# Kernel tuning notes

Measured on AMD Instinct MI355X. Metric: run time of the kernel, lower is better.

## Reference

```python
import jax, jax.numpy as jnp
import numpy as np

B, L_IN, C_IN, C_SKIP, C_OUT, DEPTH = 8, 512, 512, 512, 512, 4
D_INNER, D_STATE, D_CONV, DT_RANK = 1024, 16, 4, 32
EPS = 1e-5


def rmsnorm(x, w):
    return x * jax.lax.rsqrt(jnp.mean(x * x, axis=-1, keepdims=True) + EPS) * w


def layernorm(x, w, b):
    m = jnp.mean(x, axis=-1, keepdims=True)
    v = jnp.mean((x - m) ** 2, axis=-1, keepdims=True)
    return (x - m) * jax.lax.rsqrt(v + EPS) * w + b


def selective_scan(u, dt, A, Bm, Cm, Dp):
    # u, dt: (B, L, Di); A: (Di, N); Bm, Cm: (B, L, N); Dp: (Di,)
    def step(h, inp):
        dt_t, B_t, C_t, u_t = inp  # (B,Di),(B,N),(B,N),(B,Di)
        dA = jnp.exp(dt_t[..., None] * A)            # (B,Di,N)
        h = dA * h + (dt_t * u_t)[..., None] * B_t[:, None, :]
        y = jnp.einsum('bdn,bn->bd', h, C_t)
        return h, y

    Bb, L, Di = u.shape
    h0 = jnp.zeros((Bb, Di, A.shape[1]), u.dtype)
    xs = (dt.transpose(1, 0, 2), Bm.transpose(1, 0, 2),
          Cm.transpose(1, 0, 2), u.transpose(1, 0, 2))
    _, ys = jax.lax.scan(step, h0, xs)               # ys: (L,B,Di)
    return ys.transpose(1, 0, 2) + u * Dp


def mamba_block(x, in_w, cw, cb, xp_w, dtw, dtb, A_log, Dp, ow, ob):
    xz = x @ in_w.T                                   # (B,L,2*Di)
    xc, z = jnp.split(xz, 2, axis=-1)
    # causal depthwise conv, kernel D_CONV
    xc_t = jax.lax.conv_general_dilated(
        xc.transpose(0, 2, 1), cw[:, None, :], (1,), [(D_CONV - 1, 0)],
        feature_group_count=D_INNER,
        dimension_numbers=('NCH', 'OIH', 'NCH'))
    xc = jax.nn.silu((xc_t + cb[None, :, None]).transpose(0, 2, 1))
    xdbc = xc @ xp_w.T                                # (B,L,DT_RANK+2N)
    dtp = xdbc[..., :DT_RANK]
    Bm = xdbc[..., DT_RANK:DT_RANK + D_STATE]
    Cm = xdbc[..., DT_RANK + D_STATE:]
    dt = jax.nn.softplus(dtp @ dtw.T + dtb)
    A = -jnp.exp(A_log)
    y = selective_scan(xc, dt, A, Bm, Cm, Dp)
    return (y * jax.nn.silu(z)) @ ow.T + ob


def forward(motion_input, skip_feats, embed, w_up, b_up, w1, b1, rms_w, w2, b2,
            ln_w, ln_b, in_proj_w, conv_w, conv_b, x_proj_w, dt_proj_w,
            dt_proj_b, A_log, D_param, out_proj_w, out_proj_b,
            norm_f_w, norm_f_b):
    Bb, Lin, C = motion_input.shape
    # ConvTranspose1d(C, C, kernel=2, stride=2): non-overlapping expansion
    up = jnp.einsum('blc,cok->blko', motion_input, w_up)
    up = up.reshape(Bb, Lin * 2, C) + b_up            # (B, 2L, C)
    x = jnp.concatenate([up, skip_feats], axis=-1)    # (B, 2L, C+skip)
    # MLP: Linear -> RMSNorm -> SiLU -> Linear
    x = jax.nn.silu(rmsnorm(x @ w1.T + b1, rms_w)) @ w2.T + b2
    # MotionMamba: add embed, depth residual mamba blocks, final norm
    x = x + embed[:, None, :]
    for i in range(DEPTH):
        x = x + mamba_block(layernorm(x, ln_w[i], ln_b[i]), in_proj_w[i],
                            conv_w[i], conv_b[i], x_proj_w[i], dt_proj_w[i],
                            dt_proj_b[i], A_log[i], D_param[i],
                            out_proj_w[i], out_proj_b[i])
    return layernorm(x, norm_f_w, norm_f_b)


def setup_inputs():
    key = jax.random.key(0)
    ks = jax.random.split(key, 16)
    f = lambda k, sh: jax.random.normal(k, sh, jnp.float32) * 0.02
    inp = {}
    inp['motion_input'] = jax.random.normal(ks[0], (B, L_IN, C_IN), jnp.float32)
    inp['skip_feats'] = jax.random.normal(ks[1], (B, 2 * L_IN, C_SKIP), jnp.float32)
    inp['embed'] = jax.random.normal(ks[2], (B, C_OUT), jnp.float32)
    inp['w_up'] = f(ks[3], (C_IN, C_IN, 2))
    inp['b_up'] = jnp.zeros((C_IN,), jnp.float32)
    inp['w1'] = f(ks[4], (C_OUT, C_IN + C_SKIP))
    inp['b1'] = jnp.zeros((C_OUT,), jnp.float32)
    inp['rms_w'] = jnp.ones((C_OUT,), jnp.float32)
    inp['w2'] = f(ks[5], (C_OUT, C_OUT))
    inp['b2'] = jnp.zeros((C_OUT,), jnp.float32)
    inp['ln_w'] = jnp.ones((DEPTH, C_OUT), jnp.float32)
    inp['ln_b'] = jnp.zeros((DEPTH, C_OUT), jnp.float32)
    inp['in_proj_w'] = f(ks[6], (DEPTH, 2 * D_INNER, C_OUT))
    inp['conv_w'] = f(ks[7], (DEPTH, D_INNER, D_CONV))
    inp['conv_b'] = jnp.zeros((DEPTH, D_INNER), jnp.float32)
    inp['x_proj_w'] = f(ks[8], (DEPTH, DT_RANK + 2 * D_STATE, D_INNER))
    inp['dt_proj_w'] = f(ks[9], (DEPTH, D_INNER, DT_RANK))
    inp['dt_proj_b'] = jnp.full((DEPTH, D_INNER), -4.0, jnp.float32)
    inp['A_log'] = jnp.log(jnp.tile(jnp.arange(1, D_STATE + 1, dtype=jnp.float32), (DEPTH, D_INNER, 1)))
    inp['D_param'] = jnp.ones((DEPTH, D_INNER), jnp.float32)
    inp['out_proj_w'] = f(ks[10], (DEPTH, C_OUT, D_INNER))
    inp['out_proj_b'] = jnp.zeros((DEPTH, C_OUT), jnp.float32)
    inp['norm_f_w'] = jnp.ones((C_OUT,), jnp.float32)
    inp['norm_f_b'] = jnp.zeros((C_OUT,), jnp.float32)
    return inp


def reference(motion_input, skip_feats, embed, w_up, b_up, w1, b1, rms_w, w2,
              b2, ln_w, ln_b, in_proj_w, conv_w, conv_b, x_proj_w, dt_proj_w,
              dt_proj_b, A_log, D_param, out_proj_w, out_proj_b,
              norm_f_w, norm_f_b):
    return forward(motion_input, skip_feats, embed, w_up, b_up, w1, b1, rms_w,
                   w2, b2, ln_w, ln_b, in_proj_w, conv_w, conv_b, x_proj_w,
                   dt_proj_w, dt_proj_b, A_log, D_param, out_proj_w,
                   out_proj_b, norm_f_w, norm_f_b)
```

## Files before the change

kernel.cpp:

```cpp
#include <hip/hip_runtime.h>
#include <cstdint>
#include <cstddef>

#define DEV_INLINE __device__ __forceinline__

static constexpr float EPS = 1e-5f;

DEV_INLINE float sigmoidf_(float x) { return 1.0f / (1.0f + __expf(-x)); }
DEV_INLINE float siluf_(float x) { return x * sigmoidf_(x); }
DEV_INLINE float softplus_fast(float x) {
    return fmaxf(x, 0.0f) + __logf(1.0f + __expf(-fabsf(x)));
}
DEV_INLINE unsigned short f2bf(float x) {
    unsigned u = __builtin_bit_cast(unsigned, x);
    u += 0x7FFFu + ((u >> 16) & 1u);
    return (unsigned short)(u >> 16);
}
DEV_INLINE float bf2f(unsigned short s) {
    unsigned u = ((unsigned)s) << 16;
    return __builtin_bit_cast(float, u);
}

typedef __attribute__((ext_vector_type(8))) short bf16x8;
typedef __attribute__((ext_vector_type(4))) float f32x4;

DEV_INLINE void gload16(const unsigned short* src, char* ldsdst) {
    __builtin_amdgcn_global_load_lds(
        (const __attribute__((address_space(1))) unsigned int*)src,
        (__attribute__((address_space(3))) unsigned int*)ldsdst, 16, 0, 0);
}

DEV_INLINE void cvt8(const float* __restrict__ s, unsigned short* __restrict__ d, int t) {
    float4 f0 = *(const float4*)(s + (size_t)t * 8);
    float4 f1 = *(const float4*)(s + (size_t)t * 8 + 4);
    union { unsigned short u[8]; uint4 v; } pk;
    pk.u[0] = f2bf(f0.x); pk.u[1] = f2bf(f0.y); pk.u[2] = f2bf(f0.z); pk.u[3] = f2bf(f0.w);
    pk.u[4] = f2bf(f1.x); pk.u[5] = f2bf(f1.y); pk.u[6] = f2bf(f1.z); pk.u[7] = f2bf(f1.w);
    *(uint4*)(d + (size_t)t * 8) = pk.v;
}

__global__ __launch_bounds__(256) void cvt_bf16(
    const float* __restrict__ s, unsigned short* __restrict__ d, int n8)
{
    int t = blockIdx.x * 256 + (int)threadIdx.x;
    if (t >= n8) return;
    cvt8(s, d, t);
}

__global__ __launch_bounds__(256) void transpose_wup_bf(
    const float* __restrict__ wup, unsigned short* __restrict__ wt)
{
    int t = blockIdx.x * 256 + (int)threadIdx.x;
    if (t >= 512 * 512) return;
    int c = t >> 9, o = t & 511;
    float2 v = *(const float2*)(wup + (size_t)t * 2);
    wt[(size_t)o * 512 + c] = f2bf(v.x);
    wt[262144 + (size_t)o * 512 + c] = f2bf(v.y);
}

__global__ __launch_bounds__(256) void prep_w(
    const float* __restrict__ in_proj_w,
    const float* __restrict__ out_proj_w,
    const float* __restrict__ x_proj_w,
    const float* __restrict__ dt_proj_w,
    unsigned short* __restrict__ ipw,
    unsigned short* __restrict__ opw,
    unsigned short* __restrict__ xpw,
    unsigned short* __restrict__ wdt32)
{
    int bid = (int)blockIdx.x, tid = (int)threadIdx.x;
    if (bid < 16) {
        cvt8(dt_proj_w, wdt32, bid * 256 + tid);
    } else if (bid < 528) {
        cvt8(in_proj_w, ipw, (bid - 16) * 256 + tid);
    } else if (bid < 784) {
        cvt8(out_proj_w, opw, (bid - 528) * 256 + tid);
    } else {
        cvt8(x_proj_w, xpw, (bid - 784) * 256 + tid);
    }
}

template <int ACT, bool ACC, bool EMBED, bool OBF>
__global__ __launch_bounds__(256) void gemm_mfma(
    const unsigned short* __restrict__ A, int lda,
    const unsigned short* __restrict__ W, int ldw,
    void* __restrict__ Cv, int ldc, int N, int K, int gx,
    const float* __restrict__ bias, const float* __restrict__ embed)
{
    __shared__ unsigned short Asm[2][128 * 64];
    __shared__ unsigned short Wsm[2][128 * 64];
    const int tid = (int)threadIdx.x;
    const int lane = tid & 63;
    const int wv = tid >> 6;
    const int wm = wv >> 1, wn = wv & 1;

    const int nwg = (int)gridDim.x;
    const int lin = (int)blockIdx.x;
    const int logical = (lin & 7) * (nwg >> 3) + (lin >> 3);
    const int by = logical / gx;
    const int bx = logical - by * gx;
    const int bm = by * 128, bn = bx * 128;

    f32x4 acc[4][4] = {};

    const int l8 = lane >> 3;
    const int wc = lane & 7;
    const int wcg = wc ^ l8;

    const int NT = K >> 6;

    {
        char* aB = (char*)Asm[0];
        char* bB = (char*)Wsm[0];
#pragma unroll
        for (int i = 0; i < 4; ++i) {
            int rb = (i * 4 + wv) * 8;
            gload16(W + (size_t)(bn + rb + l8) * ldw + wcg * 8, bB + rb * 128);
            gload16(A + (size_t)(bm + rb + l8) * lda + wcg * 8, aB + rb * 128);
        }
    }
    __syncthreads();

    for (int t = 0; t < NT; ++t) {
        const int cur = t & 1;
        if (t + 1 < NT) {
            const int k1 = (t + 1) << 6;
            char* aB = (char*)Asm[cur ^ 1];
            char* bB = (char*)Wsm[cur ^ 1];
#pragma unroll
            for (int i = 0; i < 4; ++i) {
                int rb = (i * 4 + wv) * 8;
                gload16(W + (size_t)(bn + rb + l8) * ldw + k1 + wcg * 8, bB + rb * 128);
                gload16(A + (size_t)(bm + rb + l8) * lda + k1 + wcg * 8, aB + rb * 128);
            }
        }
        const char* aB = (const char*)Asm[cur];
        const char* bB = (const char*)Wsm[cur];
        const int rA = wm * 64 + (lane & 15);
        const int rB = wn * 64 + (lane & 15);
        const int q = lane >> 4;
#pragma unroll
        for (int kk = 0; kk < 2; ++kk) {
            bf16x8 af[4], bfr[4];
#pragma unroll
            for (int mi = 0; mi < 4; ++mi) {
                int row = rA + mi * 16;
                int ch = (kk * 4 + q) ^ (row & 7);
                af[mi] = *(const bf16x8*)(aB + row * 128 + ch * 16);
            }
#pragma unroll
            for (int ni = 0; ni < 4; ++ni) {
                int row = rB + ni * 16;
                int ch = (kk * 4 + q) ^ (row & 7);
                bfr[ni] = *(const bf16x8*)(bB + row * 128 + ch * 16);
            }
#pragma unroll
            for (int mi = 0; mi < 4; ++mi)
#pragma unroll
                for (int ni = 0; ni < 4; ++ni)
                    acc[mi][ni] = __builtin_amdgcn_mfma_f32_16x16x32_bf16(
                        af[mi], bfr[ni], acc[mi][ni], 0, 0, 0);
        }
        __syncthreads();
    }

    const int cn = lane & 15;
    const int r0 = (lane >> 4) * 4;
    const int eb = EMBED ? (bm >> 10) * N : 0;
#pragma unroll
    for (int ni = 0; ni < 4; ++ni) {
        int col = bn + wn * 64 + ni * 16 + cn;
        float add = bias ? bias[col] : 0.0f;
        if (EMBED) add += embed[eb + col];
#pragma unroll
        for (int mi = 0; mi < 4; ++mi) {
#pragma unroll
            for (int r = 0; r < 4; ++r) {
                int row = bm + wm * 64 + mi * 16 + r0 + r;
                float v = acc[mi][ni][r] + add;
                if (ACT == 1) v = softplus_fast(v);
                if (OBF) {
                    ((unsigned short*)Cv)[(size_t)row * ldc + col] = f2bf(v);
                } else {
                    float* p = (float*)Cv + (size_t)row * ldc + col;
                    if (ACC) *p += v; else *p = v;
                }
            }
        }
    }
}

template <int ACT, bool ACC, bool EMBED, bool OBF>
__global__ __launch_bounds__(256) void gemm_mfma64(
    const unsigned short* __restrict__ A, int lda,
    const unsigned short* __restrict__ W, int ldw,
    void* __restrict__ Cv, int ldc, int N, int K, int gx,
    const float* __restrict__ bias, const float* __restrict__ embed)
{
    __shared__ unsigned short Asm[2][64 * 64];
    __shared__ unsigned short Wsm[2][64 * 64];
    const int tid = (int)threadIdx.x;
    const int lane = tid & 63;
    const int wv = tid >> 6;
    const int wm = wv >> 1, wn = wv & 1;

    const int nwg = (int)gridDim.x;
    const int lin = (int)blockIdx.x;
    const int logical = (lin & 7) * (nwg >> 3) + (lin >> 3);
    const int by = logical / gx;
    const int bx = logical - by * gx;
    const int bm = by * 64, bn = bx * 64;

    f32x4 acc[2][2] = {};

    const int l8 = lane >> 3;
    const int wc = lane & 7;
    const int wcg = wc ^ l8;

    const int NT = K >> 6;

    {
        char* aB = (char*)Asm[0];
        char* bB = (char*)Wsm[0];
#pragma unroll
        for (int i = 0; i < 2; ++i) {
            int rb = (i * 4 + wv) * 8;
            gload16(W + (size_t)(bn + rb + l8) * ldw + wcg * 8, bB + rb * 128);
            gload16(A + (size_t)(bm + rb + l8) * lda + wcg * 8, aB + rb * 128);
        }
    }
    __syncthreads();

    for (int t = 0; t < NT; ++t) {
        const int cur = t & 1;
        if (t + 1 < NT) {
            const int k1 = (t + 1) << 6;
            char* aB = (char*)Asm[cur ^ 1];
            char* bB = (char*)Wsm[cur ^ 1];
#pragma unroll
            for (int i = 0; i < 2; ++i) {
                int rb = (i * 4 + wv) * 8;
                gload16(W + (size_t)(bn + rb + l8) * ldw + k1 + wcg * 8, bB + rb * 128);
                gload16(A + (size_t)(bm + rb + l8) * lda + k1 + wcg * 8, aB + rb * 128);
            }
        }
        const char* aB = (const char*)Asm[cur];
        const char* bB = (const char*)Wsm[cur];
        const int rA = wm * 32 + (lane & 15);
        const int rB = wn * 32 + (lane & 15);
        const int q = lane >> 4;
#pragma unroll
        for (int kk = 0; kk < 2; ++kk) {
            bf16x8 af[2], bfr[2];
#pragma unroll
            for (int mi = 0; mi < 2; ++mi) {
                int row = rA + mi * 16;
                int ch = (kk * 4 + q) ^ (row & 7);
                af[mi] = *(const bf16x8*)(aB + row * 128 + ch * 16);
            }
#pragma unroll
            for (int ni = 0; ni < 2; ++ni) {
                int row = rB + ni * 16;
                int ch = (kk * 4 + q) ^ (row & 7);
                bfr[ni] = *(const bf16x8*)(bB + row * 128 + ch * 16);
            }
#pragma unroll
            for (int mi = 0; mi < 2; ++mi)
#pragma unroll
                for (int ni = 0; ni < 2; ++ni)
                    acc[mi][ni] = __builtin_amdgcn_mfma_f32_16x16x32_bf16(
                        af[mi], bfr[ni], acc[mi][ni], 0, 0, 0);
        }
        __syncthreads();
    }

    const int cn = lane & 15;
    const int r0 = (lane >> 4) * 4;
    const int eb = EMBED ? (bm >> 10) * N : 0;
#pragma unroll
    for (int ni = 0; ni < 2; ++ni) {
        int col = bn + wn * 32 + ni * 16 + cn;
        float add = bias ? bias[col] : 0.0f;
        if (EMBED) add += embed[eb + col];
#pragma unroll
        for (int mi = 0; mi < 2; ++mi) {
#pragma unroll
            for (int r = 0; r < 4; ++r) {
                int row = bm + wm * 32 + mi * 16 + r0 + r;
                float v = acc[mi][ni][r] + add;
                if (ACT == 1) v = softplus_fast(v);
                if (OBF) {
                    ((unsigned short*)Cv)[(size_t)row * ldc + col] = f2bf(v);
                } else {
                    float* p = (float*)Cv + (size_t)row * ldc + col;
                    if (ACC) *p += v; else *p = v;
                }
            }
        }
    }
}

__global__ __launch_bounds__(256) void gemm_dt(
    const unsigned short* __restrict__ xdbc,
    const unsigned short* __restrict__ wdt,
    const float* __restrict__ bias,
    unsigned short* __restrict__ out)
{
    __shared__ unsigned short S[128 * 136];
    const int tid = (int)threadIdx.x;
    const int lane = tid & 63;
    const int wv = tid >> 6;
    const int wm = wv >> 1, wn = wv & 1;

    const int lin = (int)blockIdx.x;
    const int logical = (lin & 7) * 64 + (lin >> 3);
    const int bm = (logical >> 3) * 128;
    const int bn = (logical & 7) * 128;

    const int fr = lane & 15;
    const int q = lane >> 4;

    bf16x8 af[4], wf[4];
#pragma unroll
    for (int mi = 0; mi < 4; ++mi)
        af[mi] = *(const bf16x8*)(xdbc + (size_t)(bm + wm * 64 + mi * 16 + fr) * 64 + q * 8);
#pragma unroll
    for (int ni = 0; ni < 4; ++ni)
        wf[ni] = *(const bf16x8*)(wdt + (size_t)(bn + wn * 64 + ni * 16 + fr) * 32 + q * 8);

    f32x4 acc[4][4] = {};
#pragma unroll
    for (int mi = 0; mi < 4; ++mi)
#pragma unroll
        for (int ni = 0; ni < 4; ++ni)
            acc[mi][ni] = __builtin_amdgcn_mfma_f32_16x16x32_bf16(
                af[mi], wf[ni], acc[mi][ni], 0, 0, 0);

    const int cn = lane & 15;
    const int r0 = (lane >> 4) * 4;
#pragma unroll
    for (int ni = 0; ni < 4; ++ni) {
        int lcol = wn * 64 + ni * 16 + cn;
        float add = bias[bn + lcol];
#pragma unroll
        for (int mi = 0; mi < 4; ++mi) {
#pragma unroll
            for (int r = 0; r < 4; ++r) {
                int lrow = wm * 64 + mi * 16 + r0 + r;
                S[lrow * 136 + lcol] = f2bf(softplus_fast(acc[mi][ni][r] + add));
            }
        }
    }
    __syncthreads();

    const int row = tid >> 1;
    const int half = tid & 1;
    const unsigned short* src = S + row * 136 + half * 64;
    unsigned short* dst = out + (size_t)(bm + row) * 1024 + bn + half * 64;
#pragma unroll
    for (int k = 0; k < 8; ++k) {
        uint4 v = *(const uint4*)(src + k * 8);
        *(uint4*)(dst + k * 8) = v;
    }
}

__global__ __launch_bounds__(128) void gemm_xdbc(
    const unsigned short* __restrict__ A,
    const unsigned short* __restrict__ W,
    unsigned short* __restrict__ C)
{
    __shared__ unsigned short Asm[64 * 64];
    __shared__ unsigned short Wsm[64 * 64];
    const int tid = (int)threadIdx.x;
    const int lane = tid & 63;
    const int w = tid >> 6;
    const int bm = blockIdx.x * 64;
    const int l8 = lane >> 3, wc = lane & 7, wcg = wc ^ l8;
    char* aB = (char*)Asm;
    char* bB = (char*)Wsm;

    f32x4 acc[2][4] = {};

    for (int k0 = 0; k0 < 1024; k0 += 64) {
#pragma unroll
        for (int i = 0; i < 4; ++i) {
            int rb = (i * 2 + w) * 8;
            gload16(A + (size_t)(bm + rb + l8) * 1024 + k0 + wcg * 8, aB + rb * 128);
            gload16(W + (size_t)(rb + l8) * 1024 + k0 + wcg * 8, bB + rb * 128);
        }
        __syncthreads();
        const int rA = w * 32 + (lane & 15);
        const int rB = (lane & 15);
        const int q = lane >> 4;
#pragma unroll
        for (int kk = 0; kk < 2; ++kk) {
            bf16x8 af[2], bfr[4];
#pragma unroll
            for (int mi = 0; mi < 2; ++mi) {
                int row = rA + mi * 16;
                int ch = (kk * 4 + q) ^ (row & 7);
                af[mi] = *(const bf16x8*)(aB + row * 128 + ch * 16);
            }
#pragma unroll
            for (int ni = 0; ni < 4; ++ni) {
                int row = rB + ni * 16;
                int ch = (kk * 4 + q) ^ (row & 7);
                bfr[ni] = *(const bf16x8*)(bB + row * 128 + ch * 16);
            }
#pragma unroll
            for (int mi = 0; mi < 2; ++mi)
#pragma unroll
                for (int ni = 0; ni < 4; ++ni)
                    acc[mi][ni] = __builtin_amdgcn_mfma_f32_16x16x32_bf16(
                        af[mi], bfr[ni], acc[mi][ni], 0, 0, 0);
        }
        __syncthreads();
    }
    const int cn = lane & 15;
    const int r0 = (lane >> 4) * 4;
#pragma unroll
    for (int mi = 0; mi < 2; ++mi)
#pragma unroll
        for (int ni = 0; ni < 4; ++ni)
#pragma unroll
            for (int r = 0; r < 4; ++r) {
                int row = bm + w * 32 + mi * 16 + r0 + r;
                C[(size_t)row * 64 + ni * 16 + cn] = f2bf(acc[mi][ni][r]);
            }
}

__global__ __launch_bounds__(256) void concat_skip(
    const float* __restrict__ skip, unsigned short* __restrict__ x0)
{
    int t = blockIdx.x * 256 + (int)threadIdx.x;
    int row = t >> 6;
    int c8 = (t & 63) << 3;
    const float* s = skip + (size_t)row * 512 + c8;
    float4 f0 = *(const float4*)s;
    float4 f1 = *(const float4*)(s + 4);
    union { unsigned short u[8]; uint4 v; } pk;
    pk.u[0] = f2bf(f0.x); pk.u[1] = f2bf(f0.y); pk.u[2] = f2bf(f0.z); pk.u[3] = f2bf(f0.w);
    pk.u[4] = f2bf(f1.x); pk.u[5] = f2bf(f1.y); pk.u[6] = f2bf(f1.z); pk.u[7] = f2bf(f1.w);
    *(uint4*)(x0 + (size_t)row * 1024 + 512 + c8) = pk.v;
}

template <bool BFOUT>
__global__ __launch_bounds__(256) void layernorm_k(
    const float* __restrict__ x, void* __restrict__ outp,
    const float* __restrict__ w, const float* __restrict__ b)
{
    const int row = blockIdx.x * 4 + ((int)threadIdx.x >> 6);
    const int lane = (int)threadIdx.x & 63;
    const float* xr = x + (size_t)row * 512;
    float4 v0 = *(const float4*)(xr + lane * 4);
    float4 v1 = *(const float4*)(xr + 256 + lane * 4);
    float s = v0.x + v0.y + v0.z + v0.w + v1.x + v1.y + v1.z + v1.w;
    float q = v0.x*v0.x + v0.y*v0.y + v0.z*v0.z + v0.w*v0.w
            + v1.x*v1.x + v1.y*v1.y + v1.z*v1.z + v1.w*v1.w;
#pragma unroll
    for (int o = 32; o; o >>= 1) {
        s += __shfl_xor(s, o, 64);
        q += __shfl_xor(q, o, 64);
    }
    const float mean = s * (1.0f / 512.0f);
    const float var = q * (1.0f / 512.0f) - mean * mean;
    const float rstd = rsqrtf(var + EPS);
    float4 w0 = *(const float4*)(w + lane * 4);
    float4 w1 = *(const float4*)(w + 256 + lane * 4);
    float4 b0 = *(const float4*)(b + lane * 4);
    float4 b1 = *(const float4*)(b + 256 + lane * 4);
    float4 o0, o1;
    o0.x = (v0.x - mean) * rstd * w0.x + b0.x;
    o0.y = (v0.y - mean) * rstd * w0.y + b0.y;
    o0.z = (v0.z - mean) * rstd * w0.z + b0.z;
    o0.w = (v0.w - mean) * rstd * w0.w + b0.w;
    o1.x = (v1.x - mean) * rstd * w1.x + b1.x;
    o1.y = (v1.y - mean) * rstd * w1.y + b1.y;
    o1.z = (v1.z - mean) * rstd * w1.z + b1.z;
    o1.w = (v1.w - mean) * rstd * w1.w + b1.w;
    if (BFOUT) {
        unsigned short* ob = (unsigned short*)outp + (size_t)row * 512;
        union { unsigned short u[4]; uint2 v; } p0, p1;
        p0.u[0] = f2bf(o0.x); p0.u[1] = f2bf(o0.y); p0.u[2] = f2bf(o0.z); p0.u[3] = f2bf(o0.w);
        p1.u[0] = f2bf(o1.x); p1.u[1] = f2bf(o1.y); p1.u[2] = f2bf(o1.z); p1.u[3] = f2bf(o1.w);
        *(uint2*)(ob + lane * 4) = p0.v;
        *(uint2*)(ob + 256 + lane * 4) = p1.v;
    } else {
        float* orow = (float*)outp + (size_t)row * 512;
        *(float4*)(orow + lane * 4) = o0;
        *(float4*)(orow + 256 + lane * 4) = o1;
    }
}

__global__ __launch_bounds__(256) void rms_silu_k(
    const float* __restrict__ x, unsigned short* __restrict__ o,
    const float* __restrict__ w)
{
    const int row = blockIdx.x * 4 + ((int)threadIdx.x >> 6);
    const int lane = (int)threadIdx.x & 63;
    const float* xr = x + (size_t)row * 512;
    float4 v0 = *(const float4*)(xr + lane * 4);
    float4 v1 = *(const float4*)(xr + 256 + lane * 4);
    float q = v0.x*v0.x + v0.y*v0.y + v0.z*v0.z + v0.w*v0.w
            + v1.x*v1.x + v1.y*v1.y + v1.z*v1.z + v1.w*v1.w;
#pragma unroll
    for (int of = 32; of; of >>= 1) q += __shfl_xor(q, of, 64);
    const float scale = rsqrtf(q * (1.0f / 512.0f) + EPS);
    float4 w0 = *(const float4*)(w + lane * 4);
    float4 w1 = *(const float4*)(w + 256 + lane * 4);
    union { unsigned short u[4]; uint2 v; } p0, p1;
    p0.u[0] = f2bf(siluf_(v0.x * scale * w0.x));
    p0.u[1] = f2bf(siluf_(v0.y * scale * w0.y));
    p0.u[2] = f2bf(siluf_(v0.z * scale * w0.z));
    p0.u[3] = f2bf(siluf_(v0.w * scale * w0.w));
    p1.u[0] = f2bf(siluf_(v1.x * scale * w1.x));
    p1.u[1] = f2bf(siluf_(v1.y * scale * w1.y));
    p1.u[2] = f2bf(siluf_(v1.z * scale * w1.z));
    p1.u[3] = f2bf(siluf_(v1.w * scale * w1.w));
    unsigned short* ob = o + (size_t)row * 512;
    *(uint2*)(ob + lane * 4) = p0.v;
    *(uint2*)(ob + 256 + lane * 4) = p1.v;
}

__global__ __launch_bounds__(256) void conv_silu_k2(
    const unsigned short* __restrict__ xz, unsigned short* __restrict__ ub,
    const float* __restrict__ cw, const float* __restrict__ cb)
{
    int t = blockIdx.x * 256 + (int)threadIdx.x;
    int d = t & 1023;
    int bc = t >> 10;
    int b = bc >> 4, ch = bc & 15;
    int l0 = ch * 64;
    float4 w4 = *(const float4*)(cw + (size_t)d * 4);
    float bias = cb[d];
    const unsigned short* src = xz + ((size_t)(b * 1024 + l0)) * 2048 + d;
    unsigned short* dst = ub + ((size_t)(b * 1024 + l0)) * 1024 + d;
    float x0 = 0.f, x1 = 0.f, x2 = 0.f;
    if (l0 > 0) {
        x0 = bf2f(src[-(size_t)3 * 2048]);
        x1 = bf2f(src[-(size_t)2 * 2048]);
        x2 = bf2f(src[-(size_t)1 * 2048]);
    }
    for (int l = 0; l < 64; ++l) {
        float x3 = bf2f(src[(size_t)l * 2048]);
        float v = fmaf(x0, w4.x, fmaf(x1, w4.y, fmaf(x2, w4.z, fmaf(x3, w4.w, bias))));
        dst[(size_t)l * 1024] = f2bf(siluf_(v));
        x0 = x1; x1 = x2; x2 = x3;
    }
}

template <int CTRL>
DEV_INLINE float dpp_f(float x) {
    int yi = __builtin_amdgcn_update_dpp(
        0, __builtin_bit_cast(int, x), CTRL, 0xF, 0xF, true);
    return __builtin_bit_cast(float, yi);
}

template <int PHASE>
__global__ __launch_bounds__(256) void scan4(
    const unsigned short* __restrict__ dtp,
    const unsigned short* ubf,
    unsigned short* ybf,
    const unsigned short* __restrict__ xdbc,
    const unsigned short* __restrict__ zbf,
    float* __restrict__ hp,
    const float* __restrict__ A_log,
    const float* __restrict__ Dp)
{
    __shared__ float SDT[32][132];
    __shared__ float SB[32][20];
    __shared__ float SC[PHASE == 2 ? 32 : 1][20];
    __shared__ float YS[PHASE == 2 ? 32 : 1][68];

    const int lin = (int)blockIdx.x;
    const int logical = (lin & 7) * 128 + (lin >> 3);
    const int gg = logical & 15;
    const int rr0 = logical >> 4;
    const int c = rr0 & 7, b = rr0 >> 3;
    if (PHASE == 1 && c == 7) return;
    const int tid = (int)threadIdx.x;
    const int dl = tid >> 2, q = tid & 3;
    const int dblk = gg << 6;
    const int d = dblk + dl;
    const int m0 = b * 1024 + c * 128;

    float An[4];
#pragma unroll
    for (int j = 0; j < 4; ++j)
        An[j] = -__expf(A_log[(size_t)d * 16 + q * 4 + j]);

    float h[4] = {};
    float prod[4] = {1.f, 1.f, 1.f, 1.f};
    if (PHASE == 2) {
        const float* hpb = hp + ((size_t)(b * 1024 + d)) * 256 + q * 8;
        for (int cc = 0; cc < c; ++cc) {
            float4 v0 = *(const float4*)(hpb + cc * 32);
            float4 v1 = *(const float4*)(hpb + cc * 32 + 4);
            h[0] = fmaf(v0.y, h[0], v0.x);
            h[1] = fmaf(v0.w, h[1], v0.z);
            h[2] = fmaf(v1.y, h[2], v1.x);
            h[3] = fmaf(v1.w, h[3], v1.z);
        }
    }

    const int sr = tid >> 3;
    const int c8 = tid & 7;
    const int bcr = (tid & 127) >> 2;
    const int bne = (tid & 3) << 2;

    for (int s = 0; s < 4; ++s) {
        const int lbase = s * 32;
        {
            size_t gr = (size_t)(m0 + lbase + sr);
            uint4 d8 = *(const uint4*)(dtp + gr * 1024 + dblk + c8 * 8);
            uint4 u8 = *(const uint4*)(ubf + gr * 1024 + dblk + c8 * 8);
            const unsigned* dw = (const unsigned*)&d8;
            const unsigned* uw = (const unsigned*)&u8;
#pragma unroll
            for (int k = 0; k < 4; ++k) {
                float dt0 = bf2f((unsigned short)(dw[k] & 0xffff));
                float dt1 = bf2f((unsigned short)(dw[k] >> 16));
                float uu0 = bf2f((unsigned short)(uw[k] & 0xffff));
                float uu1 = bf2f((unsigned short)(uw[k] >> 16));
                float4 wv = {dt0, dt0 * uu0, dt1, dt1 * uu1};
                *(float4*)&SDT[sr][c8 * 16 + k * 4] = wv;
            }
        }
        {
            size_t gr = (size_t)(m0 + lbase + bcr);
            if (tid < 128) {
                uint2 Bu = *(const uint2*)(xdbc + gr * 64 + 32 + bne);
                SB[bcr][bne + 0] = bf2f((unsigned short)(Bu.x & 0xffff));
                SB[bcr][bne + 1] = bf2f((unsigned short)(Bu.x >> 16));
                SB[bcr][bne + 2] = bf2f((unsigned short)(Bu.y & 0xffff));
                SB[bcr][bne + 3] = bf2f((unsigned short)(Bu.y >> 16));
            } else if (PHASE == 2) {
                uint2 Cu = *(const uint2*)(xdbc + gr * 64 + 48 + bne);
                SC[bcr][bne + 0] = bf2f((unsigned short)(Cu.x & 0xffff));
                SC[bcr][bne + 1] = bf2f((unsigned short)(Cu.x >> 16));
                SC[bcr][bne + 2] = bf2f((unsigned short)(Cu.y & 0xffff));
                SC[bcr][bne + 3] = bf2f((unsigned short)(Cu.y >> 16));
            }
        }
        __syncthreads();

        for (int l = 0; l < 32; ++l) {
            float2 dd = *(const float2*)&SDT[l][2 * dl];
            float4 Bv = *(const float4*)&SB[l][q * 4];
            float p = 0.0f;
            float4 Cv;
            if (PHASE == 2) Cv = *(const float4*)&SC[l][q * 4];
            const float* Bp = (const float*)&Bv;
            const float* Cp = (const float*)&Cv;
#pragma unroll
            for (int j = 0; j < 4; ++j) {
                float e = __expf(dd.x * An[j]);
                if (PHASE == 1) prod[j] *= e;
                h[j] = fmaf(e, h[j], dd.y * Bp[j]);
                if (PHASE == 2) p = fmaf(h[j], Cp[j], p);
            }
            if (PHASE == 2) {
                p += dpp_f<0xB1>(p);
                p += dpp_f<0x4E>(p);
                if (q == 0) YS[l][dl] = p;
            }
        }
        __syncthreads();

        if (PHASE == 2) {
#pragma unroll
            for (int j2 = 0; j2 < 2; ++j2) {
                int task = tid + j2 * 256;
                int rw = task >> 4;
                int e4 = (task & 15) << 2;
                size_t gr = (size_t)(m0 + lbase + rw);
                float4 p4 = *(const float4*)&YS[rw][e4];
                uint2 uu = *(const uint2*)(ubf + gr * 1024 + dblk + e4);
                uint2 zz = *(const uint2*)(zbf + gr * 2048 + 1024 + dblk + e4);
                float4 Dv = *(const float4*)(Dp + dblk + e4);
                float y0 = fmaf(bf2f((unsigned short)(uu.x & 0xffff)), Dv.x, p4.x)
                         * siluf_(bf2f((unsigned short)(zz.x & 0xffff)));
                float y1 = fmaf(bf2f((unsigned short)(uu.x >> 16)), Dv.y, p4.y)
                         * siluf_(bf2f((unsigned short)(zz.x >> 16)));
                float y2 = fmaf(bf2f((unsigned short)(uu.y & 0xffff)), Dv.z, p4.z)
                         * siluf_(bf2f((unsigned short)(zz.y & 0xffff)));
                float y3 = fmaf(bf2f((unsigned short)(uu.y >> 16)), Dv.w, p4.w)
                         * siluf_(bf2f((unsigned short)(zz.y >> 16)));
                union { unsigned short u[4]; uint2 v; } pk;
                pk.u[0] = f2bf(y0); pk.u[1] = f2bf(y1);
                pk.u[2] = f2bf(y2); pk.u[3] = f2bf(y3);
                *(uint2*)(ybf + gr * 1024 + dblk + e4) = pk.v;
            }
        }
    }

    if (PHASE == 1) {
        float* hpo = hp + ((size_t)(b * 1024 + d)) * 256 + c * 32 + q * 8;
        float4 o0 = {h[0], prod[0], h[1], prod[1]};
        float4 o1 = {h[2], prod[2], h[3], prod[3]};
        *(float4*)hpo = o0;
        *(float4*)(hpo + 4) = o1;
    }
}

extern "C" void kernel_launch(void* const* d_in, const int* in_sizes, int n_in,
                              void* d_out, int out_size, void* d_ws, size_t ws_size,
                              hipStream_t stream)
{
    const float* motion     = (const float*)d_in[0];
    const float* skip       = (const float*)d_in[1];
    const float* embed      = (const float*)d_in[2];
    const float* w_up       = (const float*)d_in[3];
    const float* b_up       = (const float*)d_in[4];
    const float* w1         = (const float*)d_in[5];
    const float* b1         = (const float*)d_in[6];
    const float* rms_w      = (const float*)d_in[7];
    const float* w2         = (const float*)d_in[8];
    const float* b2         = (const float*)d_in[9];
    const float* ln_w       = (const float*)d_in[10];
    const float* ln_b       = (const float*)d_in[11];
    const float* in_proj_w  = (const float*)d_in[12];
    const float* conv_w     = (const float*)d_in[13];
    const float* conv_b     = (const float*)d_in[14];
    const float* x_proj_w   = (const float*)d_in[15];
    const float* dt_proj_w  = (const float*)d_in[16];
    const float* dt_proj_b  = (const float*)d_in[17];
    const float* A_log      = (const float*)d_in[18];
    const float* D_param    = (const float*)d_in[19];
    const float* out_proj_w = (const float*)d_in[20];
    const float* out_proj_b = (const float*)d_in[21];
    const float* norm_f_w   = (const float*)d_in[22];
    const float* norm_f_b   = (const float*)d_in[23];
    float* out = (float*)d_out;
    float* ws = (float*)d_ws;

    float* xbuf = ws;
    float* xlnf = ws + 4194304;
    unsigned short* xzbf  = (unsigned short*)(ws + 8388608);
    unsigned short* ubf   = (unsigned short*)(ws + 16777216);
    unsigned short* dtybf = (unsigned short*)(ws + 20971520);
    unsigned short* xdbc  = (unsigned short*)(ws + 25165824);
    float* hp  = ws + 25427968;
    unsigned short* xsbf = (unsigned short*)(ws + 27525120);
    unsigned short* mbf  = (unsigned short*)(ws + 29622272);
    unsigned short* ipw  = (unsigned short*)(ws + 30670848);
    unsigned short* wdt32= (unsigned short*)(ws + 31195136);
    unsigned short* opw  = (unsigned short*)(ws + 31227904);
    unsigned short* xpw  = (unsigned short*)(ws + 31490048);

    unsigned short* x0bf = xzbf;

    dim3 blk(256);

    cvt_bf16<<<dim3(1024), blk, 0, stream>>>(motion, mbf, 262144);
    transpose_wup_bf<<<dim3(1024), blk, 0, stream>>>(w_up, ipw);
    for (int k = 0; k < 2; ++k) {
        gemm_mfma64<0, false, false, true><<<dim3(1024), blk, 0, stream>>>(
            mbf, 512, ipw + (size_t)k * 262144, 512,
            x0bf + (size_t)k * 1024, 2048, 512, 512, 8, b_up, nullptr);
    }
    concat_skip<<<dim3(2048), blk, 0, stream>>>(skip, x0bf);

    cvt_bf16<<<dim3(256), blk, 0, stream>>>(w1, ipw, 65536);
    gemm_mfma64<0, false, false, false><<<dim3(1024), blk, 0, stream>>>(
        x0bf, 1024, ipw, 1024, xlnf, 512, 512, 1024, 8, b1, nullptr);
    rms_silu_k<<<dim3(2048), blk, 0, stream>>>(xlnf, xsbf, rms_w);

    cvt_bf16<<<dim3(128), blk, 0, stream>>>(w2, ipw, 32768);
    gemm_mfma64<0, false, true, false><<<dim3(1024), blk, 0, stream>>>(
        xsbf, 512, ipw, 512, xbuf, 512, 512, 512, 8, b2, embed);

    for (int i = 0; i < 4; ++i) {
        layernorm_k<true><<<dim3(2048), blk, 0, stream>>>(
            xbuf, xsbf, ln_w + (size_t)i * 512, ln_b + (size_t)i * 512);
        prep_w<<<dim3(816), blk, 0, stream>>>(
            in_proj_w + (size_t)i * 1048576, out_proj_w + (size_t)i * 524288,
            x_proj_w + (size_t)i * 65536, dt_proj_w + (size_t)i * 32768,
            ipw, opw, xpw, wdt32);
        gemm_mfma<0, false, false, true><<<dim3(1024), blk, 0, stream>>>(
            xsbf, 512, ipw, 512, xzbf, 2048, 2048, 512, 16, nullptr, nullptr);
        conv_silu_k2<<<dim3(512), blk, 0, stream>>>(
            xzbf, ubf, conv_w + (size_t)i * 4096, conv_b + (size_t)i * 1024);
        gemm_xdbc<<<dim3(128), dim3(128), 0, stream>>>(ubf, xpw, xdbc);
        gemm_dt<<<dim3(512), blk, 0, stream>>>(
            xdbc, wdt32, dt_proj_b + (size_t)i * 1024, dtybf);
        scan4<1><<<dim3(1024), blk, 0, stream>>>(
            dtybf, ubf, nullptr, xdbc, xzbf, hp,
            A_log + (size_t)i * 16384, D_param + (size_t)i * 1024);
        scan4<2><<<dim3(1024), blk, 0, stream>>>(
            dtybf, ubf, ubf, xdbc, xzbf, hp,
            A_log + (size_t)i * 16384, D_param + (size_t)i * 1024);
        gemm_mfma64<0, true, false, false><<<dim3(1024), blk, 0, stream>>>(
            ubf, 1024, opw, 1024, xbuf, 512, 512, 1024, 8,
            out_proj_b + (size_t)i * 512, nullptr);
    }

    layernorm_k<false><<<dim3(2048), blk, 0, stream>>>(xbuf, out, norm_f_w, norm_f_b);
}
```

Baseline: 738.2 us.

## Batch all weight conversions into one kernel and split scan into finer chunks

```diff
diff --git a/kernel.cpp b/kernel.cpp
--- a/kernel.cpp
+++ b/kernel.cpp
@@ -39,44 +39,45 @@
     *(uint4*)(d + (size_t)t * 8) = pk.v;
 }
 
-__global__ __launch_bounds__(256) void cvt_bf16(
-    const float* __restrict__ s, unsigned short* __restrict__ d, int n8)
-{
-    int t = blockIdx.x * 256 + (int)threadIdx.x;
-    if (t >= n8) return;
-    cvt8(s, d, t);
-}
-
-__global__ __launch_bounds__(256) void transpose_wup_bf(
-    const float* __restrict__ wup, unsigned short* __restrict__ wt)
-{
-    int t = blockIdx.x * 256 + (int)threadIdx.x;
-    if (t >= 512 * 512) return;
-    int c = t >> 9, o = t & 511;
-    float2 v = *(const float2*)(wup + (size_t)t * 2);
-    wt[(size_t)o * 512 + c] = f2bf(v.x);
-    wt[262144 + (size_t)o * 512 + c] = f2bf(v.y);
-}
-
-__global__ __launch_bounds__(256) void prep_w(
-    const float* __restrict__ in_proj_w,
-    const float* __restrict__ out_proj_w,
-    const float* __restrict__ x_proj_w,
-    const float* __restrict__ dt_proj_w,
-    unsigned short* __restrict__ ipw,
-    unsigned short* __restrict__ opw,
-    unsigned short* __restrict__ xpw,
-    unsigned short* __restrict__ wdt32)
+__global__ __launch_bounds__(256) void prep_all(
+    const float* __restrict__ motion, const float* __restrict__ wup,
+    const float* __restrict__ w1, const float* __restrict__ w2,
+    const float* __restrict__ in_proj_w, const float* __restrict__ out_proj_w,
+    const float* __restrict__ x_proj_w, const float* __restrict__ dt_proj_w,
+    unsigned short* __restrict__ mbf, unsigned short* __restrict__ wupT,
+    unsigned short* __restrict__ w1b, unsigned short* __restrict__ w2b,
+    unsigned short* __restrict__ lw)
 {
     int bid = (int)blockIdx.x, tid = (int)threadIdx.x;
-    if (bid < 16) {
-        cvt8(dt_proj_w, wdt32, bid * 256 + tid);
-    } else if (bid < 528) {
-        cvt8(in_proj_w, ipw, (bid - 16) * 256 + tid);
-    } else if (bid < 784) {
-        cvt8(out_proj_w, opw, (bid - 528) * 256 + tid);
+    if (bid < 1024) {
+        cvt8(motion, mbf, bid * 256 + tid);
+    } else if (bid < 2048) {
+        int t = (bid - 1024) * 256 + tid;
+        int c = t >> 9, o = t & 511;
+        float2 v = *(const float2*)(wup + (size_t)t * 2);
+        wupT[(size_t)o * 512 + c] = f2bf(v.x);
+        wupT[262144 + (size_t)o * 512 + c] = f2bf(v.y);
+    } else if (bid < 2304) {
+        cvt8(w1, w1b, (bid - 2048) * 256 + tid);
+    } else if (bid < 2432) {
+        cvt8(w2, w2b, (bid - 2304) * 256 + tid);
     } else {
-        cvt8(x_proj_w, xpw, (bid - 784) * 256 + tid);
+        int r = bid - 2432;
+        int layer = r / 816;
+        int lb = r - layer * 816;
+        unsigned short* base = lw + (size_t)layer * 1671168;
+        if (lb < 512) {
+            cvt8(in_proj_w + (size_t)layer * 1048576, base, lb * 256 + tid);
+        } else if (lb < 768) {
+            cvt8(out_proj_w + (size_t)layer * 524288, base + 1048576,
+                 (lb - 512) * 256 + tid);
+        } else if (lb < 800) {
+            cvt8(x_proj_w + (size_t)layer * 65536, base + 1572864,
+                 (lb - 768) * 256 + tid);
+        } else {
+            cvt8(dt_proj_w + (size_t)layer * 32768, base + 1638400,
+                 (lb - 800) * 256 + tid);
+        }
     }
 }
 
@@ -102,11 +103,9 @@
     const int bm = by * 128, bn = bx * 128;
 
     f32x4 acc[4][4] = {};
-
     const int l8 = lane >> 3;
     const int wc = lane & 7;
     const int wcg = wc ^ l8;
-
     const int NT = K >> 6;
 
     {
@@ -190,7 +189,7 @@
     }
 }
 
-template <int ACT, bool ACC, bool EMBED, bool OBF>
+template <int ACT, bool ACC, bool EMBED, bool OBF, bool UPS>
 __global__ __launch_bounds__(256) void gemm_mfma64(
     const unsigned short* __restrict__ A, int lda,
     const unsigned short* __restrict__ W, int ldw,
@@ -212,11 +211,9 @@
     const int bm = by * 64, bn = bx * 64;
 
     f32x4 acc[2][2] = {};
-
     const int l8 = lane >> 3;
     const int wc = lane & 7;
     const int wcg = wc ^ l8;
-
     const int NT = K >> 6;
 
     {
@@ -280,7 +277,7 @@
 #pragma unroll
     for (int ni = 0; ni < 2; ++ni) {
         int col = bn + wn * 32 + ni * 16 + cn;
-        float add = bias ? bias[col] : 0.0f;
+        float add = bias ? bias[UPS ? (col & 511) : col] : 0.0f;
         if (EMBED) add += embed[eb + col];
 #pragma unroll
         for (int mi = 0; mi < 2; ++mi) {
@@ -289,7 +286,10 @@
                 int row = bm + wm * 32 + mi * 16 + r0 + r;
                 float v = acc[mi][ni][r] + add;
                 if (ACT == 1) v = softplus_fast(v);
-                if (OBF) {
+                if (UPS) {
+                    size_t ad = (size_t)row * 2048 + ((col >> 9) << 10) + (col & 511);
+                    ((unsigned short*)Cv)[ad] = f2bf(v);
+                } else if (OBF) {
                     ((unsigned short*)Cv)[(size_t)row * ldc + col] = f2bf(v);
                 } else {
                     float* p = (float*)Cv + (size_t)row * ldc + col;
@@ -557,7 +557,7 @@
 }
 
 template <int PHASE>
-__global__ __launch_bounds__(256) void scan4(
+__global__ __launch_bounds__(256) void scan5(
     const unsigned short* __restrict__ dtp,
     const unsigned short* ubf,
     unsigned short* ybf,
@@ -567,33 +567,34 @@
     const float* __restrict__ A_log,
     const float* __restrict__ Dp)
 {
-    __shared__ float SDT[32][132];
+    __shared__ float SDT2[16][260];
     __shared__ float SB[32][20];
     __shared__ float SC[PHASE == 2 ? 32 : 1][20];
     __shared__ float YS[PHASE == 2 ? 32 : 1][68];
 
     const int lin = (int)blockIdx.x;
-    const int logical = (lin & 7) * 128 + (lin >> 3);
+    const int logical = (lin & 7) * 256 + (lin >> 3);
     const int gg = logical & 15;
-    const int rr0 = logical >> 4;
-    const int c = rr0 & 7, b = rr0 >> 3;
-    if (PHASE == 1 && c == 7) return;
+    const int t2 = logical >> 4;
+    const int ch = t2 & 15, b = t2 >> 4;
+    if (PHASE == 1 && ch == 15) return;
     const int tid = (int)threadIdx.x;
-    const int dl = tid >> 2, q = tid & 3;
+    const int dl = tid >> 2, q = tid & 2 ? (tid & 3) : (tid & 3);
+    const int qq = tid & 3;
     const int dblk = gg << 6;
     const int d = dblk + dl;
-    const int m0 = b * 1024 + c * 128;
+    const int m0 = b * 1024 + ch * 64;
 
     float An[4];
 #pragma unroll
     for (int j = 0; j < 4; ++j)
-        An[j] = -__expf(A_log[(size_t)d * 16 + q * 4 + j]);
+        An[j] = -__expf(A_log[(size_t)d * 16 + qq * 4 + j]);
 
     float h[4] = {};
     float prod[4] = {1.f, 1.f, 1.f, 1.f};
     if (PHASE == 2) {
-        const float* hpb = hp + ((size_t)(b * 1024 + d)) * 256 + q * 8;
-        for (int cc = 0; cc < c; ++cc) {
+        const float* hpb = hp + (((size_t)(b * 1024 + d)) * 16) * 32 + qq * 8;
+        for (int cc = 0; cc < ch; ++cc) {
             float4 v0 = *(const float4*)(hpb + cc * 32);
             float4 v1 = *(const float4*)(hpb + cc * 32 + 4);
             h[0] = fmaf(v0.y, h[0], v0.x);
@@ -603,99 +604,118 @@
         }
     }
 
-    const int sr = tid >> 3;
-    const int c8 = tid & 7;
+    const int sl2 = tid >> 4;
+    const int sdg = (tid & 15) * 4;
     const int bcr = (tid & 127) >> 2;
     const int bne = (tid & 3) << 2;
 
-    for (int s = 0; s < 4; ++s) {
+    for (int s = 0; s < 2; ++s) {
         const int lbase = s * 32;
         {
-            size_t gr = (size_t)(m0 + lbase + sr);
-            uint4 d8 = *(const uint4*)(dtp + gr * 1024 + dblk + c8 * 8);
-            uint4 u8 = *(const uint4*)(ubf + gr * 1024 + dblk + c8 * 8);
-            const unsigned* dw = (const unsigned*)&d8;
-            const unsigned* uw = (const unsigned*)&u8;
-#pragma unroll
-            for (int k = 0; k < 4; ++k) {
-                float dt0 = bf2f((unsigned short)(dw[k] & 0xffff));
-                float dt1 = bf2f((unsigned short)(dw[k] >> 16));
-                float uu0 = bf2f((unsigned short)(uw[k] & 0xffff));
-                float uu1 = bf2f((unsigned short)(uw[k] >> 16));
-                float4 wv = {dt0, dt0 * uu0, dt1, dt1 * uu1};
-                *(float4*)&SDT[sr][c8 * 16 + k * 4] = wv;
+            size_t r0 = (size_t)(m0 + lbase + 2 * sl2);
+            uint2 dA = *(const uint2*)(dtp + r0 * 1024 + dblk + sdg);
+            uint2 dB = *(const uint2*)(dtp + (r0 + 1) * 1024 + dblk + sdg);
+            uint2 uA = *(const uint2*)(ubf + r0 * 1024 + dblk + sdg);
+            uint2 uB = *(const uint2*)(ubf + (r0 + 1) * 1024 + dblk + sdg);
+            const unsigned short* da = (const unsigned short*)&dA;
+            const unsigned short* db = (const unsigned short*)&dB;
+            const unsigned short* ua = (const unsigned short*)&uA;
+            const unsigned short* ub2 = (const unsigned short*)&uB;
+#pragma unroll
+            for (int j = 0; j < 4; ++j) {
+                float d0 = bf2f(da[j]), d1 = bf2f(db[j]);
+                float4 wv = {d0, d0 * bf2f(ua[j]), d1, d1 * bf2f(ub2[j])};
+                *(float4*)&SDT2[sl2][(sdg + j) * 4] = wv;
             }
         }
         {
             size_t gr = (size_t)(m0 + lbase + bcr);
             if (tid < 128) {
                 uint2 Bu = *(const uint2*)(xdbc + gr * 64 + 32 + bne);
-                SB[bcr][bne + 0] = bf2f((unsigned short)(Bu.x & 0xffff));
-                SB[bcr][bne + 1] = bf2f((unsigned short)(Bu.x >> 16));
-                SB[bcr][bne + 2] = bf2f((unsigned short)(Bu.y & 0xffff));
-                SB[bcr][bne + 3] = bf2f((unsigned short)(Bu.y >> 16));
+                const unsigned short* bb = (const unsigned short*)&Bu;
+                float4 bv = {bf2f(bb[0]), bf2f(bb[1]), bf2f(bb[2]), bf2f(bb[3])};
+                *(float4*)&SB[bcr][bne] = bv;
             } else if (PHASE == 2) {
                 uint2 Cu = *(const uint2*)(xdbc + gr * 64 + 48 + bne);
-                SC[bcr][bne + 0] = bf2f((unsigned short)(Cu.x & 0xffff));
-                SC[bcr][bne + 1] = bf2f((unsigned short)(Cu.x >> 16));
-                SC[bcr][bne + 2] = bf2f((unsigned short)(Cu.y & 0xffff));
-                SC[bcr][bne + 3] = bf2f((unsigned short)(Cu.y >> 16));
+                const unsigned short* cc2 = (const unsigned short*)&Cu;
+                float4 cv = {bf2f(cc2[0]), bf2f(cc2[1]), bf2f(cc2[2]), bf2f(cc2[3])};
+                *(float4*)&SC[bcr][bne] = cv;
             }
         }
         __syncthreads();
 
-        for (int l = 0; l < 32; ++l) {
-            float2 dd = *(const float2*)&SDT[l][2 * dl];
-            float4 Bv = *(const float4*)&SB[l][q * 4];
-            float p = 0.0f;
-            float4 Cv;
-            if (PHASE == 2) Cv = *(const float4*)&SC[l][q * 4];
-            const float* Bp = (const float*)&Bv;
-            const float* Cp = (const float*)&Cv;
+        for (int l2 = 0; l2 < 16; ++l2) {
+            float4 sd = *(const float4*)&SDT2[l2][dl * 4];
+            float4 B0 = *(const float4*)&SB[2 * l2][qq * 4];
+            float4 B1 = *(const float4*)&SB[2 * l2 + 1][qq * 4];
+            float p0 = 0.0f, p1 = 0.0f;
+            float4 C0, C1;
+            if (PHASE == 2) {
+                C0 = *(const float4*)&SC[2 * l2][qq * 4];
+                C1 = *(const float4*)&SC[2 * l2 + 1][qq * 4];
+            }
+            const float* B0p = (const float*)&B0;
+            const float* B1p = (const float*)&B1;
+            const float* C0p = (const float*)&C0;
+            const float* C1p = (const float*)&C1;
 #pragma unroll
             for (int j = 0; j < 4; ++j) {
-                float e = __expf(dd.x * An[j]);
-                if (PHASE == 1) prod[j] *= e;
-                h[j] = fmaf(e, h[j], dd.y * Bp[j]);
-                if (PHASE == 2) p = fmaf(h[j], Cp[j], p);
+                float e0 = __expf(sd.x * An[j]);
+                if (PHASE == 1) prod[j] *= e0;
+                h[j] = fmaf(e0, h[j], sd.y * B0p[j]);
+                if (PHASE == 2) p0 = fmaf(h[j], C0p[j], p0);
+                float e1 = __expf(sd.z * An[j]);
+                if (PHASE == 1) prod[j] *= e1;
+                h[j] = fmaf(e1, h[j], sd.w * B1p[j]);
+                if (PHASE == 2) p1 = fmaf(h[j], C1p[j], p1);
             }
             if (PHASE == 2) {
-                p += dpp_f<0xB1>(p);
-                p += dpp_f<0x4E>(p);
-                if (q == 0) YS[l][dl] = p;
+                p0 += dpp_f<0xB1>(p0);
+                p0 += dpp_f<0x4E>(p0);
+                p1 += dpp_f<0xB1>(p1);
+                p1 += dpp_f<0x4E>(p1);
+                if (qq == 0) {
+                    YS[2 * l2][dl] = p0;
+                    YS[2 * l2 + 1][dl] = p1;
+                }
             }
         }
         __syncthreads();
 
         if (PHASE == 2) {
-#pragma unroll
-            for (int j2 = 0; j2 < 2; ++j2) {
-                int task = tid + j2 * 256;
-                int rw = task >> 4;
-                int e4 = (task & 15) << 2;
-                size_t gr = (size_t)(m0 + lbase + rw);
-                float4 p4 = *(const float4*)&YS[rw][e4];
-                uint2 uu = *(const uint2*)(ubf + gr * 1024 + dblk + e4);
-                uint2 zz = *(const uint2*)(zbf + gr * 2048 + 1024 + dblk + e4);
-                float4 Dv = *(const float4*)(Dp + dblk + e4);
-                float y0 = fmaf(bf2f((unsigned short)(uu.x & 0xffff)), Dv.x, p4.x)
-                         * siluf_(bf2f((unsigned short)(zz.x & 0xffff)));
-                float y1 = fmaf(bf2f((unsigned short)(uu.x >> 16)), Dv.y, p4.y)
-                         * siluf_(bf2f((unsigned short)(zz.x >> 16)));
-                float y2 = fmaf(bf2f((unsigned short)(uu.y & 0xffff)), Dv.z, p4.z)
-                         * siluf_(bf2f((unsigned short)(zz.y & 0xffff)));
-                float y3 = fmaf(bf2f((unsigned short)(uu.y >> 16)), Dv.w, p4.w)
-                         * siluf_(bf2f((unsigned short)(zz.y >> 16)));
-                union { unsigned short u[4]; uint2 v; } pk;
-                pk.u[0] = f2bf(y0); pk.u[1] = f2bf(y1);
-                pk.u[2] = f2bf(y2); pk.u[3] = f2bf(y3);
-                *(uint2*)(ybf + gr * 1024 + dblk + e4) = pk.v;
-            }
-        }
+            const int row = tid >> 3;
+            const int e8 = (tid & 7) * 8;
+            size_t gr = (size_t)(m0 + lbase + row);
+            float4 p40 = *(const float4*)&YS[row][e8];
+            float4 p41 = *(const float4*)&YS[row][e8 + 4];
+            uint4 uu = *(const uint4*)(ubf + gr * 1024 + dblk + e8);
+            uint4 zz = *(const uint4*)(zbf + gr * 2048 + 1024 + dblk + e8);
+            float4 D0 = *(const float4*)(Dp + dblk + e8);
+            float4 D1 = *(const float4*)(Dp + dblk + e8 + 4);
+            const unsigned short* up = (const unsigned short*)&uu;
+            const unsigned short* zp = (const unsigned short*)&zz;
+            const float* pp0 = (const float*)&p40;
+            const float* pp1 = (const float*)&p41;
+            const float* dd0 = (const float*)&D0;
+            const float* dd1 = (const float*)&D1;
+            union { unsigned short u[8]; uint4 v; } pk;
+#pragma unroll
+            for (int j = 0; j < 4; ++j) {
+                float y = fmaf(bf2f(up[j]), dd0[j], pp0[j]) * siluf_(bf2f(zp[j]));
+                pk.u[j] = f2bf(y);
+            }
+#pragma unroll
+            for (int j = 0; j < 4; ++j) {
+                float y = fmaf(bf2f(up[4 + j]), dd1[j], pp1[j]) * siluf_(bf2f(zp[4 + j]));
+                pk.u[4 + j] = f2bf(y);
+            }
+            *(uint4*)(ybf + gr * 1024 + dblk + e8) = pk.v;
+        }
+        __syncthreads();
     }
 
     if (PHASE == 1) {
-        float* hpo = hp + ((size_t)(b * 1024 + d)) * 256 + c * 32 + q * 8;
+        float* hpo = hp + (((size_t)(b * 1024 + d) * 16 + ch)) * 32 + qq * 8;
         float4 o0 = {h[0], prod[0], h[1], prod[1]};
         float4 o1 = {h[2], prod[2], h[3], prod[3]};
         *(float4*)hpo = o0;
@@ -741,56 +761,53 @@
     unsigned short* dtybf = (unsigned short*)(ws + 20971520);
     unsigned short* xdbc  = (unsigned short*)(ws + 25165824);
     float* hp  = ws + 25427968;
-    unsigned short* xsbf = (unsigned short*)(ws + 27525120);
-    unsigned short* mbf  = (unsigned short*)(ws + 29622272);
-    unsigned short* ipw  = (unsigned short*)(ws + 30670848);
-    unsigned short* wdt32= (unsigned short*)(ws + 31195136);
-    unsigned short* opw  = (unsigned short*)(ws + 31227904);
-    unsigned short* xpw  = (unsigned short*)(ws + 31490048);
+    unsigned short* xsbf = (unsigned short*)(ws + 29622272);
+    unsigned short* mbf  = (unsigned short*)(ws + 31719424);
+    unsigned short* wupT = (unsigned short*)(ws + 32768000);
+    unsigned short* w1b  = (unsigned short*)(ws + 33030144);
+    unsigned short* w2b  = (unsigned short*)(ws + 33292288);
+    unsigned short* lw   = (unsigned short*)(ws + 33423360);
 
     unsigned short* x0bf = xzbf;
 
     dim3 blk(256);
 
-    cvt_bf16<<<dim3(1024), blk, 0, stream>>>(motion, mbf, 262144);
-    transpose_wup_bf<<<dim3(1024), blk, 0, stream>>>(w_up, ipw);
-    for (int k = 0; k < 2; ++k) {
-        gemm_mfma64<0, false, false, true><<<dim3(1024), blk, 0, stream>>>(
-            mbf, 512, ipw + (size_t)k * 262144, 512,
-            x0bf + (size_t)k * 1024, 2048, 512, 512, 8, b_up, nullptr);
-    }
+    prep_all<<<dim3(5696), blk, 0, stream>>>(
+        motion, w_up, w1, w2, in_proj_w, out_proj_w, x_proj_w, dt_proj_w,
+        mbf, wupT, w1b, w2b, lw);
+
+    gemm_mfma64<0, false, false, true, true><<<dim3(1024), blk, 0, stream>>>(
+        mbf, 512, wupT, 512, x0bf, 0, 1024, 512, 16, b_up, nullptr);
     concat_skip<<<dim3(2048), blk, 0, stream>>>(skip, x0bf);
 
-    cvt_bf16<<<dim3(256), blk, 0, stream>>>(w1, ipw, 65536);
-    gemm_mfma64<0, false, false, false><<<dim3(1024), blk, 0, stream>>>(
-        x0bf, 1024, ipw, 1024, xlnf, 512, 512, 1024, 8, b1, nullptr);
+    gemm_mfma64<0, false, false, false, false><<<dim3(1024), blk, 0, stream>>>(
+        x0bf, 1024, w1b, 1024, xlnf, 512, 512, 1024, 8, b1, nullptr);
     rms_silu_k<<<dim3(2048), blk, 0, stream>>>(xlnf, xsbf, rms_w);
 
-    cvt_bf16<<<dim3(128), blk, 0, stream>>>(w2, ipw, 32768);
-    gemm_mfma64<0, false, true, false><<<dim3(1024), blk, 0, stream>>>(
-        xsbf, 512, ipw, 512, xbuf, 512, 512, 512, 8, b2, embed);
+    gemm_mfma64<0, false, true, false, false><<<dim3(1024), blk, 0, stream>>>(
+        xsbf, 512, w2b, 512, xbuf, 512, 512, 512, 8, b2, embed);
 
     for (int i = 0; i < 4; ++i) {
+        unsigned short* ipw = lw + (size_t)i * 1671168;
+        unsigned short* opw = ipw + 1048576;
+        unsigned short* xpw = ipw + 1572864;
+        unsigned short* wdt = ipw + 1638400;
         layernorm_k<true><<<dim3(2048), blk, 0, stream>>>(
             xbuf, xsbf, ln_w + (size_t)i * 512, ln_b + (size_t)i * 512);
-        prep_w<<<dim3(816), blk, 0, stream>>>(
-            in_proj_w + (size_t)i * 1048576, out_proj_w + (size_t)i * 524288,
-            x_proj_w + (size_t)i * 65536, dt_proj_w + (size_t)i * 32768,
-            ipw, opw, xpw, wdt32);
         gemm_mfma<0, false, false, true><<<dim3(1024), blk, 0, stream>>>(
             xsbf, 512, ipw, 512, xzbf, 2048, 2048, 512, 16, nullptr, nullptr);
         conv_silu_k2<<<dim3(512), blk, 0, stream>>>(
             xzbf, ubf, conv_w + (size_t)i * 4096, conv_b + (size_t)i * 1024);
         gemm_xdbc<<<dim3(128), dim3(128), 0, stream>>>(ubf, xpw, xdbc);
         gemm_dt<<<dim3(512), blk, 0, stream>>>(
-            xdbc, wdt32, dt_proj_b + (size_t)i * 1024, dtybf);
-        scan4<1><<<dim3(1024), blk, 0, stream>>>(
+            xdbc, wdt, dt_proj_b + (size_t)i * 1024, dtybf);
+        scan5<1><<<dim3(2048), blk, 0, stream>>>(
             dtybf, ubf, nullptr, xdbc, xzbf, hp,
             A_log + (size_t)i * 16384, D_param + (size_t)i * 1024);
-        scan4<2><<<dim3(1024), blk, 0, stream>>>(
+        scan5<2><<<dim3(2048), blk, 0, stream>>>(
             dtybf, ubf, ubf, xdbc, xzbf, hp,
             A_log + (size_t)i * 16384, D_param + (size_t)i * 1024);
-        gemm_mfma64<0, true, false, false><<<dim3(1024), blk, 0, stream>>>(
+        gemm_mfma64<0, true, false, false, false><<<dim3(1024), blk, 0, stream>>>(
             ubf, 1024, opw, 1024, xbuf, 512, 512, 1024, 8,
             out_proj_b + (size_t)i * 512, nullptr);
     }
```

After: 692.3 us. -6.2%, faster.
